# Kernel tuning notes

Hardware: AMD Instinct MI355X
Metric: run time of the kernel (lower is better)

## Reference

```python
import jax, jax.numpy as jnp
import numpy as np

H = 5  # hidden size of both LSTMs

def _lstm_layer(x, Wih, Whh, bih, bhh):
    """x: [B,T,I] -> hs: [B,T,H]. PyTorch gate order i,f,g,o; zero init state."""
    B, T, _ = x.shape
    # precompute input contribution for all timesteps: [T,B,4H]
    xg = (jnp.einsum('bti,gi->btg', x, Wih) + bih + bhh).transpose(1, 0, 2)
    def step(carry, xg_t):
        h, c = carry
        g = xg_t + h @ Whh.T
        i, f, gg, o = jnp.split(g, 4, axis=-1)
        c = jax.nn.sigmoid(f) * c + jax.nn.sigmoid(i) * jnp.tanh(gg)
        h = jax.nn.sigmoid(o) * jnp.tanh(c)
        return (h, c), h
    h0 = jnp.zeros((B, H), x.dtype)
    (_, _), hs = jax.lax.scan(step, (h0, h0), xg)
    return hs.transpose(1, 0, 2)  # [B,T,H]

def setup_inputs() -> dict:
    key = jax.random.key(0)
    ks = jax.random.split(key, 32)
    B, T = 16384, 128
    def u(k, shape, fan):
        s = 1.0 / np.sqrt(fan)
        return jax.random.uniform(k, shape, jnp.float32, -s, s)
    inp = {
        'x1': jax.random.normal(ks[0], (B, T, 5), jnp.float32),
        'x2': jax.random.normal(ks[1], (B, T, 5), jnp.float32),
        # lstm1 (1 layer)
        'Wih1': u(ks[2], (4*H, 5), H), 'Whh1': u(ks[3], (4*H, H), H),
        'bih1': u(ks[4], (4*H,), H), 'bhh1': u(ks[5], (4*H,), H),
        # lstm2 layer 0
        'Wih2a': u(ks[6], (4*H, 5), H), 'Whh2a': u(ks[7], (4*H, H), H),
        'bih2a': u(ks[8], (4*H,), H), 'bhh2a': u(ks[9], (4*H,), H),
        # lstm2 layer 1
        'Wih2b': u(ks[10], (4*H, H), H), 'Whh2b': u(ks[11], (4*H, H), H),
        'bih2b': u(ks[12], (4*H,), H), 'bhh2b': u(ks[13], (4*H,), H),
        # FC stack 20->32->32->16->16->5
        'W1': u(ks[14], (32, 20), 20), 'b1': u(ks[15], (32,), 20),
        'W2': u(ks[16], (32, 32), 32), 'b2': u(ks[17], (32,), 32),
        'W3': u(ks[18], (16, 32), 32), 'b3': u(ks[19], (16,), 32),
        'W4': u(ks[20], (16, 16), 16), 'b4': u(ks[21], (16,), 16),
        'W5': u(ks[22], (5, 16), 16), 'b5': u(ks[23], (5,), 16),
    }
    return inp

def reference(x1, x2, Wih1, Whh1, bih1, bhh1, Wih2a, Whh2a, bih2a, bhh2a,
              Wih2b, Whh2b, bih2b, bhh2b, W1, b1, W2, b2, W3, b3, W4, b4, W5, b5):
    out1 = _lstm_layer(x1, Wih1, Whh1, bih1, bhh1)[:, -1, :]            # [B,5]
    h2 = _lstm_layer(x2, Wih2a, Whh2a, bih2a, bhh2a)                    # [B,T,5]
    out2 = _lstm_layer(h2, Wih2b, Whh2b, bih2b, bhh2b)[:, -1, :]        # [B,5]
    out = jnp.concatenate([x1[:, -1, :], x2[:, -1, :], out1, out2], axis=1)  # [B,20]
    out = jax.nn.relu(out @ W1.T + b1)
    out = jax.nn.relu(out @ W2.T + b2)
    out = jax.nn.relu(out @ W3.T + b3)
    out = jax.nn.relu(out @ W4.T + b4)
    return out @ W5.T + b5  # [B,5]
```

## Files before the change

kernel.cpp:

```cpp
#include <hip/hip_runtime.h>

#define DEV __device__ __forceinline__
#define KSIG (-1.442695041f)
#define KTANH (-2.885390082f)

DEV float fexp2(float x) { return __builtin_amdgcn_exp2f(x); }
DEV float frcp(float x) { return __builtin_amdgcn_rcpf(x); }
DEV float bperm(int a, float x) {
  return __int_as_float(__builtin_amdgcn_ds_bpermute(a, __float_as_int(x)));
}

struct CellB {
  float w[4][10];
  float b[4];
};

DEV void load_cellB(CellB& W, int u, const float* __restrict__ Wih,
                    const float* __restrict__ Whh,
                    const float* __restrict__ bih,
                    const float* __restrict__ bhh) {
#pragma unroll
  for (int rt = 0; rt < 4; ++rt) {
    int row = 5 * rt + u;
    float kx = (rt == 2) ? KTANH : KSIG;
#pragma unroll
    for (int k = 0; k < 5; ++k) {
      W.w[rt][k] = kx * Wih[row * 5 + k];
      W.w[rt][5 + k] = kx * Whh[row * 5 + k];
    }
    W.b[rt] = kx * (bih[row] + bhh[row]);
  }
}

DEV void cellB_step(const CellB& W, const float xin[5], float hAll[5],
                    float& c, const int bp[5]) {
  float acc[4];
#pragma unroll
  for (int rt = 0; rt < 4; ++rt) {
    float a = W.b[rt];
#pragma unroll
    for (int k = 0; k < 5; ++k) a = fmaf(W.w[rt][k], xin[k], a);
#pragma unroll
    for (int k = 0; k < 5; ++k) a = fmaf(W.w[rt][5 + k], hAll[k], a);
    acc[rt] = a;
  }
  float gi = frcp(1.f + fexp2(acc[0]));
  float gf = frcp(1.f + fexp2(acc[1]));
  float gg = fmaf(2.f, frcp(1.f + fexp2(acc[2])), -1.f);
  float go = frcp(1.f + fexp2(acc[3]));
  c = fmaf(gf, c, gi * gg);
  float th = fmaf(2.f, frcp(1.f + fexp2(KTANH * c)), -1.f);
  float h = go * th;
#pragma unroll
  for (int u2 = 0; u2 < 5; ++u2) hAll[u2] = bperm(bp[u2], h);
}

__global__ __launch_bounds__(64, 2) void rnn5_kernel(
    const float* __restrict__ x1, const float* __restrict__ x2,
    const float* __restrict__ Wih1, const float* __restrict__ Whh1,
    const float* __restrict__ bih1, const float* __restrict__ bhh1,
    const float* __restrict__ Wih2a, const float* __restrict__ Whh2a,
    const float* __restrict__ bih2a, const float* __restrict__ bhh2a,
    const float* __restrict__ Wih2b, const float* __restrict__ Whh2b,
    const float* __restrict__ bih2b, const float* __restrict__ bhh2b,
    const float* __restrict__ W1, const float* __restrict__ b1,
    const float* __restrict__ W2, const float* __restrict__ b2,
    const float* __restrict__ W3, const float* __restrict__ b3,
    const float* __restrict__ W4, const float* __restrict__ b4,
    const float* __restrict__ W5, const float* __restrict__ b5,
    float* __restrict__ out, int B) {
  __shared__ float sIn[12][20];
  __shared__ float sA[12][32];
  __shared__ float sB[12][32];

  const int l = threadIdx.x;
  const int g = l / 5;
  const int u = l - 5 * g;
  const bool act = (g < 12);
  const int el = act ? g : 11;
  const int eg = blockIdx.x * 12 + el;
  const int egc = (eg < B) ? eg : (B - 1);

  CellB Wc0, Wc1, Wc2;
  load_cellB(Wc0, u, Wih1, Whh1, bih1, bhh1);
  load_cellB(Wc1, u, Wih2a, Whh2a, bih2a, bhh2a);
  load_cellB(Wc2, u, Wih2b, Whh2b, bih2b, bhh2b);

  int bp[5];
#pragma unroll
  for (int u2 = 0; u2 < 5; ++u2) bp[u2] = (5 * g + u2) * 4;

  const float* px1 = x1 + (size_t)egc * 640;
  const float* px2 = x2 + (size_t)egc * 640;

  float h1[5], h2a[5], h2b[5];
  float c1 = 0.f, c2 = 0.f, c3 = 0.f;
  float xa[5], xb[5];
#pragma unroll
  for (int k = 0; k < 5; ++k) {
    h1[k] = h2a[k] = h2b[k] = 0.f;
    xa[k] = px1[k];
    xb[k] = px2[k];
  }

  for (int t = 0; t < 128; ++t) {
    const int tn = (t < 127) ? t + 1 : 127;
    float na[5], nb[5];
#pragma unroll
    for (int k = 0; k < 5; ++k) {
      na[k] = px1[tn * 5 + k];
      nb[k] = px2[tn * 5 + k];
    }
    cellB_step(Wc0, xa, h1, c1, bp);
    cellB_step(Wc1, xb, h2a, c2, bp);
    cellB_step(Wc2, h2a, h2b, c3, bp);
#pragma unroll
    for (int k = 0; k < 5; ++k) {
      xa[k] = na[k];
      xb[k] = nb[k];
    }
  }

  if (act) {
    sIn[el][u] = xa[u];
    sIn[el][5 + u] = xb[u];
    sIn[el][10 + u] = h1[u];
    sIn[el][15 + u] = h2b[u];
  }
  __syncthreads();

  for (int task = l; task < 12 * 32; task += 64) {
    int e = task >> 5, n = task & 31;
    float acc = b1[n];
#pragma unroll
    for (int k = 0; k < 20; ++k) acc = fmaf(W1[n * 20 + k], sIn[e][k], acc);
    sA[e][n] = fmaxf(acc, 0.f);
  }
  __syncthreads();
  for (int task = l; task < 12 * 32; task += 64) {
    int e = task >> 5, n = task & 31;
    float acc = b2[n];
#pragma unroll
    for (int k = 0; k < 32; ++k) acc = fmaf(W2[n * 32 + k], sA[e][k], acc);
    sB[e][n] = fmaxf(acc, 0.f);
  }
  __syncthreads();
  for (int task = l; task < 12 * 16; task += 64) {
    int e = task >> 4, n = task & 15;
    float acc = b3[n];
#pragma unroll
    for (int k = 0; k < 32; ++k) acc = fmaf(W3[n * 32 + k], sB[e][k], acc);
    sA[e][n] = fmaxf(acc, 0.f);
  }
  __syncthreads();
  for (int task = l; task < 12 * 16; task += 64) {
    int e = task >> 4, n = task & 15;
    float acc = b4[n];
#pragma unroll
    for (int k = 0; k < 16; ++k) acc = fmaf(W4[n * 16 + k], sA[e][k], acc);
    sB[e][n] = fmaxf(acc, 0.f);
  }
  __syncthreads();
  if (l < 60) {
    int e = l / 5, n = l - 5 * (l / 5);
    float acc = b5[n];
#pragma unroll
    for (int k = 0; k < 16; ++k) acc = fmaf(W5[n * 16 + k], sB[e][k], acc);
    int ego = blockIdx.x * 12 + e;
    if (ego < B) out[(size_t)ego * 5 + n] = acc;
  }
}

extern "C" void kernel_launch(void* const* d_in, const int* in_sizes, int n_in,
                              void* d_out, int out_size, void* d_ws,
                              size_t ws_size, hipStream_t stream) {
  const float* x1 = (const float*)d_in[0];
  const float* x2 = (const float*)d_in[1];
  const float* Wih1 = (const float*)d_in[2];
  const float* Whh1 = (const float*)d_in[3];
  const float* bih1 = (const float*)d_in[4];
  const float* bhh1 = (const float*)d_in[5];
  const float* Wih2a = (const float*)d_in[6];
  const float* Whh2a = (const float*)d_in[7];
  const float* bih2a = (const float*)d_in[8];
  const float* bhh2a = (const float*)d_in[9];
  const float* Wih2b = (const float*)d_in[10];
  const float* Whh2b = (const float*)d_in[11];
  const float* bih2b = (const float*)d_in[12];
  const float* bhh2b = (const float*)d_in[13];
  const float* W1 = (const float*)d_in[14];
  const float* b1 = (const float*)d_in[15];
  const float* W2 = (const float*)d_in[16];
  const float* b2 = (const float*)d_in[17];
  const float* W3 = (const float*)d_in[18];
  const float* b3 = (const float*)d_in[19];
  const float* W4 = (const float*)d_in[20];
  const float* b4 = (const float*)d_in[21];
  const float* W5 = (const float*)d_in[22];
  const float* b5 = (const float*)d_in[23];

  int B = in_sizes[0] / 640;
  int blocks = (B + 11) / 12;

  rnn5_kernel<<<blocks, 64, 0, stream>>>(
      x1, x2, Wih1, Whh1, bih1, bhh1, Wih2a, Whh2a, bih2a, bhh2a, Wih2b, Whh2b,
      bih2b, bhh2b, W1, b1, W2, b2, W3, b3, W4, b4, W5, b5, (float*)d_out, B);
}
```

Measured before the change: 241.9 us.

## Split LSTM branches into separate blocks, use packed FMA, move FC to separate kernel

The fused recurrent kernel is split so one set of blocks runs the single-layer LSTM on x1 and another set runs the two-layer stack on x2. This doubles the block count and shortens the serial per-block chain to at most two cells per step. The gate dot products now use packed two-wide FMAs. The FC stack moves to a second kernel with one element per thread, passing hidden states through the output buffer and workspace. The cost is imbalance between the two block roles, an extra launch, and a global round trip for the hidden states. fc_kernel reads wsh1 from d_out while writing out, but each thread reads its own row before writing it.

```diff
diff --git a/kernel.cpp b/kernel.cpp
--- a/kernel.cpp
+++ b/kernel.cpp
@@ -3,19 +3,24 @@
 #define DEV __device__ __forceinline__
 #define KSIG (-1.442695041f)
 #define KTANH (-2.885390082f)
+
+typedef float f2 __attribute__((ext_vector_type(2)));
 
 DEV float fexp2(float x) { return __builtin_amdgcn_exp2f(x); }
 DEV float frcp(float x) { return __builtin_amdgcn_rcpf(x); }
 DEV float bperm(int a, float x) {
   return __int_as_float(__builtin_amdgcn_ds_bpermute(a, __float_as_int(x)));
 }
-
-struct CellB {
-  float w[4][10];
-  float b[4];
+DEV f2 pkfma(f2 a, f2 b, f2 c) { return __builtin_elementwise_fma(a, b, c); }
+
+struct CellP {
+  f2 wx[4][2];
+  f2 wh[4][2];
+  float wx4[4], wh4[4];
+  f2 b2[4];
 };
 
-DEV void load_cellB(CellB& W, int u, const float* __restrict__ Wih,
+DEV void load_cellP(CellP& W, int u, const float* __restrict__ Wih,
                     const float* __restrict__ Whh,
                     const float* __restrict__ bih,
                     const float* __restrict__ bhh) {
@@ -23,26 +28,30 @@
   for (int rt = 0; rt < 4; ++rt) {
     int row = 5 * rt + u;
     float kx = (rt == 2) ? KTANH : KSIG;
-#pragma unroll
-    for (int k = 0; k < 5; ++k) {
-      W.w[rt][k] = kx * Wih[row * 5 + k];
-      W.w[rt][5 + k] = kx * Whh[row * 5 + k];
-    }
-    W.b[rt] = kx * (bih[row] + bhh[row]);
-  }
-}
-
-DEV void cellB_step(const CellB& W, const float xin[5], float hAll[5],
-                    float& c, const int bp[5]) {
+    W.wx[rt][0] = (f2){kx * Wih[row * 5 + 0], kx * Wih[row * 5 + 1]};
+    W.wx[rt][1] = (f2){kx * Wih[row * 5 + 2], kx * Wih[row * 5 + 3]};
+    W.wx4[rt] = kx * Wih[row * 5 + 4];
+    W.wh[rt][0] = (f2){kx * Whh[row * 5 + 0], kx * Whh[row * 5 + 1]};
+    W.wh[rt][1] = (f2){kx * Whh[row * 5 + 2], kx * Whh[row * 5 + 3]};
+    W.wh4[rt] = kx * Whh[row * 5 + 4];
+    W.b2[rt] = (f2){kx * (bih[row] + bhh[row]), 0.f};
+  }
+}
+
+DEV void stepP(const CellP& W, const f2 xp[2], float x4, float hAll[5],
+               float& c, const int bp[5]) {
+  f2 hp0 = (f2){hAll[0], hAll[1]};
+  f2 hp1 = (f2){hAll[2], hAll[3]};
   float acc[4];
 #pragma unroll
   for (int rt = 0; rt < 4; ++rt) {
-    float a = W.b[rt];
-#pragma unroll
-    for (int k = 0; k < 5; ++k) a = fmaf(W.w[rt][k], xin[k], a);
-#pragma unroll
-    for (int k = 0; k < 5; ++k) a = fmaf(W.w[rt][5 + k], hAll[k], a);
-    acc[rt] = a;
+    f2 a2 = pkfma(W.wx[rt][0], xp[0], W.b2[rt]);
+    a2 = pkfma(W.wx[rt][1], xp[1], a2);
+    a2 = pkfma(W.wh[rt][0], hp0, a2);
+    a2 = pkfma(W.wh[rt][1], hp1, a2);
+    float a = a2.x + a2.y;
+    a = fmaf(W.wx4[rt], x4, a);
+    acc[rt] = fmaf(W.wh4[rt], hAll[4], a);
   }
   float gi = frcp(1.f + fexp2(acc[0]));
   float gf = frcp(1.f + fexp2(acc[1]));
@@ -55,7 +64,7 @@
   for (int u2 = 0; u2 < 5; ++u2) hAll[u2] = bperm(bp[u2], h);
 }
 
-__global__ __launch_bounds__(64, 2) void rnn5_kernel(
+__global__ __launch_bounds__(64, 2) void rnn_split_kernel(
     const float* __restrict__ x1, const float* __restrict__ x2,
     const float* __restrict__ Wih1, const float* __restrict__ Whh1,
     const float* __restrict__ bih1, const float* __restrict__ bhh1,
@@ -63,111 +72,130 @@
     const float* __restrict__ bih2a, const float* __restrict__ bhh2a,
     const float* __restrict__ Wih2b, const float* __restrict__ Whh2b,
     const float* __restrict__ bih2b, const float* __restrict__ bhh2b,
-    const float* __restrict__ W1, const float* __restrict__ b1,
-    const float* __restrict__ W2, const float* __restrict__ b2,
-    const float* __restrict__ W3, const float* __restrict__ b3,
-    const float* __restrict__ W4, const float* __restrict__ b4,
-    const float* __restrict__ W5, const float* __restrict__ b5,
-    float* __restrict__ out, int B) {
-  __shared__ float sIn[12][20];
-  __shared__ float sA[12][32];
-  __shared__ float sB[12][32];
-
+    float* __restrict__ h1out, float* __restrict__ h2out, int B, int nB) {
   const int l = threadIdx.x;
   const int g = l / 5;
   const int u = l - 5 * g;
   const bool act = (g < 12);
   const int el = act ? g : 11;
-  const int eg = blockIdx.x * 12 + el;
+  const bool roleB = (blockIdx.x < (unsigned)nB);
+  const int blk = roleB ? blockIdx.x : blockIdx.x - nB;
+  const int eg = blk * 12 + el;
   const int egc = (eg < B) ? eg : (B - 1);
 
-  CellB Wc0, Wc1, Wc2;
-  load_cellB(Wc0, u, Wih1, Whh1, bih1, bhh1);
-  load_cellB(Wc1, u, Wih2a, Whh2a, bih2a, bhh2a);
-  load_cellB(Wc2, u, Wih2b, Whh2b, bih2b, bhh2b);
-
   int bp[5];
 #pragma unroll
   for (int u2 = 0; u2 < 5; ++u2) bp[u2] = (5 * g + u2) * 4;
 
-  const float* px1 = x1 + (size_t)egc * 640;
-  const float* px2 = x2 + (size_t)egc * 640;
-
-  float h1[5], h2a[5], h2b[5];
-  float c1 = 0.f, c2 = 0.f, c3 = 0.f;
-  float xa[5], xb[5];
+  if (roleB) {
+    CellP Wa, Wb;
+    load_cellP(Wa, u, Wih2a, Whh2a, bih2a, bhh2a);
+    load_cellP(Wb, u, Wih2b, Whh2b, bih2b, bhh2b);
+    const float* px = x2 + (size_t)egc * 640;
+
+    float h2a[5], h2b[5];
+    float c2 = 0.f, c3 = 0.f;
+#pragma unroll
+    for (int k = 0; k < 5; ++k) h2a[k] = h2b[k] = 0.f;
+    f2 xp[2] = {(f2){px[0], px[1]}, (f2){px[2], px[3]}};
+    float x4 = px[4];
+
+    for (int t = 0; t < 128; ++t) {
+      const int tn = (t < 127) ? t + 1 : 127;
+      f2 n0 = (f2){px[tn * 5 + 0], px[tn * 5 + 1]};
+      f2 n1 = (f2){px[tn * 5 + 2], px[tn * 5 + 3]};
+      float n4 = px[tn * 5 + 4];
+      stepP(Wa, xp, x4, h2a, c2, bp);
+      f2 hp[2] = {(f2){h2a[0], h2a[1]}, (f2){h2a[2], h2a[3]}};
+      stepP(Wb, hp, h2a[4], h2b, c3, bp);
+      xp[0] = n0;
+      xp[1] = n1;
+      x4 = n4;
+    }
+    if (act && eg < B) h2out[(size_t)eg * 5 + u] = h2b[u];
+  } else {
+    CellP W0;
+    load_cellP(W0, u, Wih1, Whh1, bih1, bhh1);
+    const float* px = x1 + (size_t)egc * 640;
+
+    float h1[5];
+    float c1 = 0.f;
+#pragma unroll
+    for (int k = 0; k < 5; ++k) h1[k] = 0.f;
+    f2 xp[2] = {(f2){px[0], px[1]}, (f2){px[2], px[3]}};
+    float x4 = px[4];
+
+    for (int t = 0; t < 128; ++t) {
+      const int tn = (t < 127) ? t + 1 : 127;
+      f2 n0 = (f2){px[tn * 5 + 0], px[tn * 5 + 1]};
+      f2 n1 = (f2){px[tn * 5 + 2], px[tn * 5 + 3]};
+      float n4 = px[tn * 5 + 4];
+      stepP(W0, xp, x4, h1, c1, bp);
+      xp[0] = n0;
+      xp[1] = n1;
+      x4 = n4;
+    }
+    if (act && eg < B) h1out[(size_t)eg * 5 + u] = h1[u];
+  }
+}
+
+__global__ __launch_bounds__(64) void fc_kernel(
+    const float* __restrict__ x1, const float* __restrict__ x2,
+    const float* wsh1, const float* __restrict__ wsh2,
+    const float* __restrict__ W1, const float* __restrict__ b1,
+    const float* __restrict__ W2, const float* __restrict__ b2,
+    const float* __restrict__ W3, const float* __restrict__ b3,
+    const float* __restrict__ W4, const float* __restrict__ b4,
+    const float* __restrict__ W5, const float* __restrict__ b5, float* out,
+    int B) {
+  int e = blockIdx.x * 64 + threadIdx.x;
+  if (e >= B) return;
+  float in0[20];
 #pragma unroll
   for (int k = 0; k < 5; ++k) {
-    h1[k] = h2a[k] = h2b[k] = 0.f;
-    xa[k] = px1[k];
-    xb[k] = px2[k];
-  }
-
-  for (int t = 0; t < 128; ++t) {
-    const int tn = (t < 127) ? t + 1 : 127;
-    float na[5], nb[5];
-#pragma unroll
-    for (int k = 0; k < 5; ++k) {
-      na[k] = px1[tn * 5 + k];
-      nb[k] = px2[tn * 5 + k];
-    }
-    cellB_step(Wc0, xa, h1, c1, bp);
-    cellB_step(Wc1, xb, h2a, c2, bp);
-    cellB_step(Wc2, h2a, h2b, c3, bp);
-#pragma unroll
-    for (int k = 0; k < 5; ++k) {
-      xa[k] = na[k];
-      xb[k] = nb[k];
-    }
-  }
-
-  if (act) {
-    sIn[el][u] = xa[u];
-    sIn[el][5 + u] = xb[u];
-    sIn[el][10 + u] = h1[u];
-    sIn[el][15 + u] = h2b[u];
-  }
-  __syncthreads();
-
-  for (int task = l; task < 12 * 32; task += 64) {
-    int e = task >> 5, n = task & 31;
+    in0[k] = x1[(size_t)e * 640 + 635 + k];
+    in0[5 + k] = x2[(size_t)e * 640 + 635 + k];
+    in0[10 + k] = wsh1[(size_t)e * 5 + k];
+    in0[15 + k] = wsh2[(size_t)e * 5 + k];
+  }
+  float v1[32];
+#pragma unroll
+  for (int n = 0; n < 32; ++n) {
     float acc = b1[n];
 #pragma unroll
-    for (int k = 0; k < 20; ++k) acc = fmaf(W1[n * 20 + k], sIn[e][k], acc);
-    sA[e][n] = fmaxf(acc, 0.f);
-  }
-  __syncthreads();
-  for (int task = l; task < 12 * 32; task += 64) {
-    int e = task >> 5, n = task & 31;
+    for (int k = 0; k < 20; ++k) acc = fmaf(W1[n * 20 + k], in0[k], acc);
+    v1[n] = fmaxf(acc, 0.f);
+  }
+  float v2[32];
+#pragma unroll
+  for (int n = 0; n < 32; ++n) {
     float acc = b2[n];
 #pragma unroll
-    for (int k = 0; k < 32; ++k) acc = fmaf(W2[n * 32 + k], sA[e][k], acc);
-    sB[e][n] = fmaxf(acc, 0.f);
-  }
-  __syncthreads();
-  for (int task = l; task < 12 * 16; task += 64) {
-    int e = task >> 4, n = task & 15;
+    for (int k = 0; k < 32; ++k) acc = fmaf(W2[n * 32 + k], v1[k], acc);
+    v2[n] = fmaxf(acc, 0.f);
+  }
+  float v3[16];
+#pragma unroll
+  for (int n = 0; n < 16; ++n) {
     float acc = b3[n];
 #pragma unroll
-    for (int k = 0; k < 32; ++k) acc = fmaf(W3[n * 32 + k], sB[e][k], acc);
-    sA[e][n] = fmaxf(acc, 0.f);
-  }
-  __syncthreads();
-  for (int task = l; task < 12 * 16; task += 64) {
-    int e = task >> 4, n = task & 15;
+    for (int k = 0; k < 32; ++k) acc = fmaf(W3[n * 32 + k], v2[k], acc);
+    v3[n] = fmaxf(acc, 0.f);
+  }
+  float v4[16];
+#pragma unroll
+  for (int n = 0; n < 16; ++n) {
     float acc = b4[n];
 #pragma unroll
-    for (int k = 0; k < 16; ++k) acc = fmaf(W4[n * 16 + k], sA[e][k], acc);
-    sB[e][n] = fmaxf(acc, 0.f);
-  }
-  __syncthreads();
-  if (l < 60) {
-    int e = l / 5, n = l - 5 * (l / 5);
+    for (int k = 0; k < 16; ++k) acc = fmaf(W4[n * 16 + k], v3[k], acc);
+    v4[n] = fmaxf(acc, 0.f);
+  }
+#pragma unroll
+  for (int n = 0; n < 5; ++n) {
     float acc = b5[n];
 #pragma unroll
-    for (int k = 0; k < 16; ++k) acc = fmaf(W5[n * 16 + k], sB[e][k], acc);
-    int ego = blockIdx.x * 12 + e;
-    if (ego < B) out[(size_t)ego * 5 + n] = acc;
+    for (int k = 0; k < 16; ++k) acc = fmaf(W5[n * 16 + k], v4[k], acc);
+    out[(size_t)e * 5 + n] = acc;
   }
 }
 
@@ -200,9 +228,14 @@
   const float* b5 = (const float*)d_in[23];
 
   int B = in_sizes[0] / 640;
-  int blocks = (B + 11) / 12;
-
-  rnn5_kernel<<<blocks, 64, 0, stream>>>(
+  int nB = (B + 11) / 12;
+  float* wsh1 = (float*)d_out;
+  float* wsh2 = (float*)d_ws;
+
+  rnn_split_kernel<<<2 * nB, 64, 0, stream>>>(
       x1, x2, Wih1, Whh1, bih1, bhh1, Wih2a, Whh2a, bih2a, bhh2a, Wih2b, Whh2b,
-      bih2b, bhh2b, W1, b1, W2, b2, W3, b3, W4, b4, W5, b5, (float*)d_out, B);
-}
+      bih2b, bhh2b, wsh1, wsh2, B, nB);
+  fc_kernel<<<(B + 63) / 64, 64, 0, stream>>>(x1, x2, wsh1, wsh2, W1, b1, W2,
+                                              b2, W3, b3, W4, b4, W5, b5,
+                                              (float*)d_out, B);
+}
```

Measured after the change: 257.5 us. 1.06x slower.

## Split the three LSTM cells across three wavefronts and use packed FMA

Applied to the files above, without the earlier changes.

Each of the three LSTM cells now runs on its own wavefront inside a 192-thread block instead of one wave running all three in sequence. The second layer of lstm2 runs one step behind, reading h2a from a double-buffered shared array, with a __syncthreads after every timestep. The gate dot products now use packed 2-wide float FMAs. The aim is to shorten each wave's serial dependency chain and raise occupancy, at the cost of 128 block barriers and lockstep coupling between the waves.

```diff
diff --git a/kernel.cpp b/kernel.cpp
--- a/kernel.cpp
+++ b/kernel.cpp
@@ -3,19 +3,24 @@
 #define DEV __device__ __forceinline__
 #define KSIG (-1.442695041f)
 #define KTANH (-2.885390082f)
+
+typedef float f2 __attribute__((ext_vector_type(2)));
 
 DEV float fexp2(float x) { return __builtin_amdgcn_exp2f(x); }
 DEV float frcp(float x) { return __builtin_amdgcn_rcpf(x); }
 DEV float bperm(int a, float x) {
   return __int_as_float(__builtin_amdgcn_ds_bpermute(a, __float_as_int(x)));
 }
-
-struct CellB {
-  float w[4][10];
-  float b[4];
+DEV f2 pkfma(f2 a, f2 b, f2 c) { return __builtin_elementwise_fma(a, b, c); }
+
+struct CellP {
+  f2 wx[4][2];
+  f2 wh[4][2];
+  float wx4[4], wh4[4];
+  f2 b2[4];
 };
 
-DEV void load_cellB(CellB& W, int u, const float* __restrict__ Wih,
+DEV void load_cellP(CellP& W, int u, const float* __restrict__ Wih,
                     const float* __restrict__ Whh,
                     const float* __restrict__ bih,
                     const float* __restrict__ bhh) {
@@ -23,26 +28,30 @@
   for (int rt = 0; rt < 4; ++rt) {
     int row = 5 * rt + u;
     float kx = (rt == 2) ? KTANH : KSIG;
-#pragma unroll
-    for (int k = 0; k < 5; ++k) {
-      W.w[rt][k] = kx * Wih[row * 5 + k];
-      W.w[rt][5 + k] = kx * Whh[row * 5 + k];
-    }
-    W.b[rt] = kx * (bih[row] + bhh[row]);
-  }
-}
-
-DEV void cellB_step(const CellB& W, const float xin[5], float hAll[5],
-                    float& c, const int bp[5]) {
+    W.wx[rt][0] = (f2){kx * Wih[row * 5 + 0], kx * Wih[row * 5 + 1]};
+    W.wx[rt][1] = (f2){kx * Wih[row * 5 + 2], kx * Wih[row * 5 + 3]};
+    W.wx4[rt] = kx * Wih[row * 5 + 4];
+    W.wh[rt][0] = (f2){kx * Whh[row * 5 + 0], kx * Whh[row * 5 + 1]};
+    W.wh[rt][1] = (f2){kx * Whh[row * 5 + 2], kx * Whh[row * 5 + 3]};
+    W.wh4[rt] = kx * Whh[row * 5 + 4];
+    W.b2[rt] = (f2){kx * (bih[row] + bhh[row]), 0.f};
+  }
+}
+
+DEV float stepP(const CellP& W, const f2 xp[2], float x4, float hAll[5],
+                float& c, const int bp[5]) {
+  f2 hp0 = (f2){hAll[0], hAll[1]};
+  f2 hp1 = (f2){hAll[2], hAll[3]};
   float acc[4];
 #pragma unroll
   for (int rt = 0; rt < 4; ++rt) {
-    float a = W.b[rt];
-#pragma unroll
-    for (int k = 0; k < 5; ++k) a = fmaf(W.w[rt][k], xin[k], a);
-#pragma unroll
-    for (int k = 0; k < 5; ++k) a = fmaf(W.w[rt][5 + k], hAll[k], a);
-    acc[rt] = a;
+    f2 a2 = pkfma(W.wx[rt][0], xp[0], W.b2[rt]);
+    a2 = pkfma(W.wx[rt][1], xp[1], a2);
+    a2 = pkfma(W.wh[rt][0], hp0, a2);
+    a2 = pkfma(W.wh[rt][1], hp1, a2);
+    float a = a2.x + a2.y;
+    a = fmaf(W.wx4[rt], x4, a);
+    acc[rt] = fmaf(W.wh4[rt], hAll[4], a);
   }
   float gi = frcp(1.f + fexp2(acc[0]));
   float gf = frcp(1.f + fexp2(acc[1]));
@@ -53,9 +62,10 @@
   float h = go * th;
 #pragma unroll
   for (int u2 = 0; u2 < 5; ++u2) hAll[u2] = bperm(bp[u2], h);
-}
-
-__global__ __launch_bounds__(64, 2) void rnn5_kernel(
+  return h;
+}
+
+__global__ __launch_bounds__(192, 4) void rnn3w_kernel(
     const float* __restrict__ x1, const float* __restrict__ x2,
     const float* __restrict__ Wih1, const float* __restrict__ Whh1,
     const float* __restrict__ bih1, const float* __restrict__ bhh1,
@@ -69,11 +79,14 @@
     const float* __restrict__ W4, const float* __restrict__ b4,
     const float* __restrict__ W5, const float* __restrict__ b5,
     float* __restrict__ out, int B) {
+  __shared__ float sH[2][64];
   __shared__ float sIn[12][20];
   __shared__ float sA[12][32];
   __shared__ float sB[12][32];
 
-  const int l = threadIdx.x;
+  const int tid = threadIdx.x;
+  const int w = tid >> 6;
+  const int l = tid & 63;
   const int g = l / 5;
   const int u = l - 5 * g;
   const bool act = (g < 12);
@@ -81,55 +94,85 @@
   const int eg = blockIdx.x * 12 + el;
   const int egc = (eg < B) ? eg : (B - 1);
 
-  CellB Wc0, Wc1, Wc2;
-  load_cellB(Wc0, u, Wih1, Whh1, bih1, bhh1);
-  load_cellB(Wc1, u, Wih2a, Whh2a, bih2a, bhh2a);
-  load_cellB(Wc2, u, Wih2b, Whh2b, bih2b, bhh2b);
+  CellP W;
+  if (w == 0)
+    load_cellP(W, u, Wih1, Whh1, bih1, bhh1);
+  else if (w == 1)
+    load_cellP(W, u, Wih2a, Whh2a, bih2a, bhh2a);
+  else
+    load_cellP(W, u, Wih2b, Whh2b, bih2b, bhh2b);
 
   int bp[5];
 #pragma unroll
   for (int u2 = 0; u2 < 5; ++u2) bp[u2] = (5 * g + u2) * 4;
 
-  const float* px1 = x1 + (size_t)egc * 640;
-  const float* px2 = x2 + (size_t)egc * 640;
-
-  float h1[5], h2a[5], h2b[5];
-  float c1 = 0.f, c2 = 0.f, c3 = 0.f;
-  float xa[5], xb[5];
-#pragma unroll
-  for (int k = 0; k < 5; ++k) {
-    h1[k] = h2a[k] = h2b[k] = 0.f;
-    xa[k] = px1[k];
-    xb[k] = px2[k];
-  }
+  const float* px = ((w == 0) ? x1 : x2) + (size_t)egc * 640;
+
+  if (tid < 128) sH[tid >> 6][tid & 63] = 0.f;
+
+  float hAll[5];
+  float c = 0.f, hOwn = 0.f;
+#pragma unroll
+  for (int k = 0; k < 5; ++k) hAll[k] = 0.f;
+
+  f2 xp[2];
+  float x4 = 0.f;
+  if (w < 2) {
+    xp[0] = (f2){px[0], px[1]};
+    xp[1] = (f2){px[2], px[3]};
+    x4 = px[4];
+  }
+  __syncthreads();
 
   for (int t = 0; t < 128; ++t) {
-    const int tn = (t < 127) ? t + 1 : 127;
-    float na[5], nb[5];
-#pragma unroll
-    for (int k = 0; k < 5; ++k) {
-      na[k] = px1[tn * 5 + k];
-      nb[k] = px2[tn * 5 + k];
-    }
-    cellB_step(Wc0, xa, h1, c1, bp);
-    cellB_step(Wc1, xb, h2a, c2, bp);
-    cellB_step(Wc2, h2a, h2b, c3, bp);
-#pragma unroll
-    for (int k = 0; k < 5; ++k) {
-      xa[k] = na[k];
-      xb[k] = nb[k];
-    }
+    f2 xin[2];
+    float xin4;
+    if (w == 2) {
+      const float* s = &sH[(t + 1) & 1][g * 5];
+      xin[0] = (f2){s[0], s[1]};
+      xin[1] = (f2){s[2], s[3]};
+      xin4 = s[4];
+    } else {
+      xin[0] = xp[0];
+      xin[1] = xp[1];
+      xin4 = x4;
+    }
+    if (w < 2) {
+      const int tn = (t < 127) ? t + 1 : 127;
+      xp[0] = (f2){px[tn * 5 + 0], px[tn * 5 + 1]};
+      xp[1] = (f2){px[tn * 5 + 2], px[tn * 5 + 3]};
+      x4 = px[tn * 5 + 4];
+    }
+    hOwn = stepP(W, xin, xin4, hAll, c, bp);
+    if (w == 2 && t == 0) {
+#pragma unroll
+      for (int k = 0; k < 5; ++k) hAll[k] = 0.f;
+      c = 0.f;
+      hOwn = 0.f;
+    }
+    if (w == 1 && act) sH[t & 1][g * 5 + u] = hOwn;
+    __syncthreads();
+  }
+
+  if (w == 2) {
+    const float* s = &sH[1][g * 5];
+    f2 xin[2] = {(f2){s[0], s[1]}, (f2){s[2], s[3]}};
+    hOwn = stepP(W, xin, s[4], hAll, c, bp);
   }
 
   if (act) {
-    sIn[el][u] = xa[u];
-    sIn[el][5 + u] = xb[u];
-    sIn[el][10 + u] = h1[u];
-    sIn[el][15 + u] = h2b[u];
-  }
-  __syncthreads();
-
-  for (int task = l; task < 12 * 32; task += 64) {
+    if (w == 0) {
+      sIn[el][u] = x1[(size_t)egc * 640 + 635 + u];
+      sIn[el][10 + u] = hOwn;
+    } else if (w == 1) {
+      sIn[el][5 + u] = x2[(size_t)egc * 640 + 635 + u];
+    } else {
+      sIn[el][15 + u] = hOwn;
+    }
+  }
+  __syncthreads();
+
+  for (int task = tid; task < 12 * 32; task += 192) {
     int e = task >> 5, n = task & 31;
     float acc = b1[n];
 #pragma unroll
@@ -137,7 +180,7 @@
     sA[e][n] = fmaxf(acc, 0.f);
   }
   __syncthreads();
-  for (int task = l; task < 12 * 32; task += 64) {
+  for (int task = tid; task < 12 * 32; task += 192) {
     int e = task >> 5, n = task & 31;
     float acc = b2[n];
 #pragma unroll
@@ -145,24 +188,24 @@
     sB[e][n] = fmaxf(acc, 0.f);
   }
   __syncthreads();
-  for (int task = l; task < 12 * 16; task += 64) {
-    int e = task >> 4, n = task & 15;
+  {
+    int e = tid >> 4, n = tid & 15;
     float acc = b3[n];
 #pragma unroll
     for (int k = 0; k < 32; ++k) acc = fmaf(W3[n * 32 + k], sB[e][k], acc);
     sA[e][n] = fmaxf(acc, 0.f);
   }
   __syncthreads();
-  for (int task = l; task < 12 * 16; task += 64) {
-    int e = task >> 4, n = task & 15;
+  {
+    int e = tid >> 4, n = tid & 15;
     float acc = b4[n];
 #pragma unroll
     for (int k = 0; k < 16; ++k) acc = fmaf(W4[n * 16 + k], sA[e][k], acc);
     sB[e][n] = fmaxf(acc, 0.f);
   }
   __syncthreads();
-  if (l < 60) {
-    int e = l / 5, n = l - 5 * (l / 5);
+  if (tid < 60) {
+    int e = tid / 5, n = tid - 5 * (tid / 5);
     float acc = b5[n];
 #pragma unroll
     for (int k = 0; k < 16; ++k) acc = fmaf(W5[n * 16 + k], sB[e][k], acc);
@@ -200,9 +243,9 @@
   const float* b5 = (const float*)d_in[23];
 
   int B = in_sizes[0] / 640;
-  int blocks = (B + 11) / 12;
-
-  rnn5_kernel<<<blocks, 64, 0, stream>>>(
+  int nB = (B + 11) / 12;
+
+  rnn3w_kernel<<<nB, 192, 0, stream>>>(
       x1, x2, Wih1, Whh1, bih1, bhh1, Wih2a, Whh2a, bih2a, bhh2a, Wih2b, Whh2b,
       bih2b, bhh2b, W1, b1, W2, b2, W3, b3, W4, b4, W5, b5, (float*)d_out, B);
 }
```

Result: faster. 224.3 us (-7.3%).

## Remap LSTM work to 4 lanes per sequence, one gate type per lane

Applied to the files above, without the earlier changes.

Each wavefront now handles 16 sequences with 4 lanes per sequence; each lane computes one gate type for all 5 hidden units. Gates are exchanged across the 4-lane quad with DPP broadcasts instead of ds_bpermute, so every lane holds the full hidden state without LDS round trips. Dot products use packed 2-wide FMAs, and 16 lanes now fill the wave instead of 60 of 64. The trade-off is redundant cell/tanh computation across the 4 lanes and higher register pressure, with launch bounds lowered to 1 block per CU hint.

```diff
diff --git a/kernel.cpp b/kernel.cpp
--- a/kernel.cpp
+++ b/kernel.cpp
@@ -4,58 +4,94 @@
 #define KSIG (-1.442695041f)
 #define KTANH (-2.885390082f)
 
+typedef float f2 __attribute__((ext_vector_type(2)));
+
 DEV float fexp2(float x) { return __builtin_amdgcn_exp2f(x); }
 DEV float frcp(float x) { return __builtin_amdgcn_rcpf(x); }
-DEV float bperm(int a, float x) {
-  return __int_as_float(__builtin_amdgcn_ds_bpermute(a, __float_as_int(x)));
-}
-
-struct CellB {
-  float w[4][10];
-  float b[4];
+DEV f2 pkfma(f2 a, f2 b, f2 c) { return __builtin_elementwise_fma(a, b, c); }
+
+template <int S>
+DEV float qb(float x) {
+  int i = __builtin_amdgcn_update_dpp(0, __float_as_int(x), S * 0x55, 0xF, 0xF,
+                                      true);
+  return __int_as_float(i);
+}
+
+struct CellQ {
+  f2 wx01[5], wx23[5], wh01[5], wh23[5];
+  float wx4[5], wh4[5], b[5];
 };
 
-DEV void load_cellB(CellB& W, int u, const float* __restrict__ Wih,
+DEV void load_cellQ(CellQ& W, int s, const float* __restrict__ Wih,
                     const float* __restrict__ Whh,
                     const float* __restrict__ bih,
                     const float* __restrict__ bhh) {
-#pragma unroll
-  for (int rt = 0; rt < 4; ++rt) {
-    int row = 5 * rt + u;
-    float kx = (rt == 2) ? KTANH : KSIG;
-#pragma unroll
-    for (int k = 0; k < 5; ++k) {
-      W.w[rt][k] = kx * Wih[row * 5 + k];
-      W.w[rt][5 + k] = kx * Whh[row * 5 + k];
-    }
-    W.b[rt] = kx * (bih[row] + bhh[row]);
-  }
-}
-
-DEV void cellB_step(const CellB& W, const float xin[5], float hAll[5],
-                    float& c, const int bp[5]) {
-  float acc[4];
-#pragma unroll
-  for (int rt = 0; rt < 4; ++rt) {
-    float a = W.b[rt];
-#pragma unroll
-    for (int k = 0; k < 5; ++k) a = fmaf(W.w[rt][k], xin[k], a);
-#pragma unroll
-    for (int k = 0; k < 5; ++k) a = fmaf(W.w[rt][5 + k], hAll[k], a);
-    acc[rt] = a;
-  }
-  float gi = frcp(1.f + fexp2(acc[0]));
-  float gf = frcp(1.f + fexp2(acc[1]));
-  float gg = fmaf(2.f, frcp(1.f + fexp2(acc[2])), -1.f);
-  float go = frcp(1.f + fexp2(acc[3]));
-  c = fmaf(gf, c, gi * gg);
-  float th = fmaf(2.f, frcp(1.f + fexp2(KTANH * c)), -1.f);
-  float h = go * th;
-#pragma unroll
-  for (int u2 = 0; u2 < 5; ++u2) hAll[u2] = bperm(bp[u2], h);
-}
-
-__global__ __launch_bounds__(64, 2) void rnn5_kernel(
+  const float kx = (s == 2) ? KTANH : KSIG;
+#pragma unroll
+  for (int j = 0; j < 5; ++j) {
+    const int row = 5 * s + j;
+    W.wx01[j] = (f2){kx * Wih[row * 5 + 0], kx * Wih[row * 5 + 1]};
+    W.wx23[j] = (f2){kx * Wih[row * 5 + 2], kx * Wih[row * 5 + 3]};
+    W.wx4[j] = kx * Wih[row * 5 + 4];
+    W.wh01[j] = (f2){kx * Whh[row * 5 + 0], kx * Whh[row * 5 + 1]};
+    W.wh23[j] = (f2){kx * Whh[row * 5 + 2], kx * Whh[row * 5 + 3]};
+    W.wh4[j] = kx * Whh[row * 5 + 4];
+    W.b[j] = kx * (bih[row] + bhh[row]);
+  }
+}
+
+struct StateQ {
+  f2 hp01, hp23;
+  float h4;
+  float c[5];
+};
+
+DEV void zeroQ(StateQ& st) {
+  st.hp01 = (f2){0.f, 0.f};
+  st.hp23 = (f2){0.f, 0.f};
+  st.h4 = 0.f;
+#pragma unroll
+  for (int j = 0; j < 5; ++j) st.c[j] = 0.f;
+}
+
+DEV void stepQ(const CellQ& W, f2 x01, f2 x23, float x4, StateQ& st, float m2,
+               float a2) {
+  float a[5];
+#pragma unroll
+  for (int j = 0; j < 5; ++j) {
+    f2 acc2 = pkfma(W.wx01[j], x01, (f2){W.b[j], 0.f});
+    acc2 = pkfma(W.wx23[j], x23, acc2);
+    acc2 = pkfma(W.wh01[j], st.hp01, acc2);
+    acc2 = pkfma(W.wh23[j], st.hp23, acc2);
+    float acc = acc2.x + acc2.y;
+    acc = fmaf(W.wx4[j], x4, acc);
+    acc = fmaf(W.wh4[j], st.h4, acc);
+    a[j] = fmaf(m2, frcp(1.f + fexp2(acc)), a2);
+  }
+#pragma unroll
+  for (int j = 0; j < 5; ++j) {
+    float I = qb<0>(a[j]);
+    float F = qb<1>(a[j]);
+    float G = qb<2>(a[j]);
+    float O = qb<3>(a[j]);
+    float cj = fmaf(F, st.c[j], I * G);
+    st.c[j] = cj;
+    float th = fmaf(2.f, frcp(1.f + fexp2(KTANH * cj)), -1.f);
+    float h = O * th;
+    if (j == 0)
+      st.hp01.x = h;
+    else if (j == 1)
+      st.hp01.y = h;
+    else if (j == 2)
+      st.hp23.x = h;
+    else if (j == 3)
+      st.hp23.y = h;
+    else
+      st.h4 = h;
+  }
+}
+
+__global__ __launch_bounds__(64, 1) void rnnq_kernel(
     const float* __restrict__ x1, const float* __restrict__ x2,
     const float* __restrict__ Wih1, const float* __restrict__ Whh1,
     const float* __restrict__ bih1, const float* __restrict__ bhh1,
@@ -69,105 +105,141 @@
     const float* __restrict__ W4, const float* __restrict__ b4,
     const float* __restrict__ W5, const float* __restrict__ b5,
     float* __restrict__ out, int B) {
-  __shared__ float sIn[12][20];
-  __shared__ float sA[12][32];
-  __shared__ float sB[12][32];
+  __shared__ float sIn[16][20];
+  __shared__ float sA[16][32];
+  __shared__ float sBf[16][32];
 
   const int l = threadIdx.x;
-  const int g = l / 5;
-  const int u = l - 5 * g;
-  const bool act = (g < 12);
-  const int el = act ? g : 11;
-  const int eg = blockIdx.x * 12 + el;
+  const int e = l >> 2;
+  const int s = l & 3;
+  const int eg = blockIdx.x * 16 + e;
   const int egc = (eg < B) ? eg : (B - 1);
 
-  CellB Wc0, Wc1, Wc2;
-  load_cellB(Wc0, u, Wih1, Whh1, bih1, bhh1);
-  load_cellB(Wc1, u, Wih2a, Whh2a, bih2a, bhh2a);
-  load_cellB(Wc2, u, Wih2b, Whh2b, bih2b, bhh2b);
-
-  int bp[5];
-#pragma unroll
-  for (int u2 = 0; u2 < 5; ++u2) bp[u2] = (5 * g + u2) * 4;
+  CellQ Wc1, Wc2a, Wc2b;
+  load_cellQ(Wc1, s, Wih1, Whh1, bih1, bhh1);
+  load_cellQ(Wc2a, s, Wih2a, Whh2a, bih2a, bhh2a);
+  load_cellQ(Wc2b, s, Wih2b, Whh2b, bih2b, bhh2b);
+
+  const float m2 = (s == 2) ? 2.f : 1.f;
+  const float a2 = (s == 2) ? -1.f : 0.f;
 
   const float* px1 = x1 + (size_t)egc * 640;
   const float* px2 = x2 + (size_t)egc * 640;
 
-  float h1[5], h2a[5], h2b[5];
-  float c1 = 0.f, c2 = 0.f, c3 = 0.f;
-  float xa[5], xb[5];
-#pragma unroll
-  for (int k = 0; k < 5; ++k) {
-    h1[k] = h2a[k] = h2b[k] = 0.f;
-    xa[k] = px1[k];
-    xb[k] = px2[k];
-  }
+  StateQ s1, s2a, s2b;
+  zeroQ(s1);
+  zeroQ(s2a);
+  zeroQ(s2b);
+
+  f2 xa01 = (f2){px1[0], px1[1]}, xa23 = (f2){px1[2], px1[3]};
+  float xa4 = px1[4];
+  f2 xb01 = (f2){px2[0], px2[1]}, xb23 = (f2){px2[2], px2[3]};
+  float xb4 = px2[4];
 
   for (int t = 0; t < 128; ++t) {
     const int tn = (t < 127) ? t + 1 : 127;
-    float na[5], nb[5];
-#pragma unroll
-    for (int k = 0; k < 5; ++k) {
-      na[k] = px1[tn * 5 + k];
-      nb[k] = px2[tn * 5 + k];
-    }
-    cellB_step(Wc0, xa, h1, c1, bp);
-    cellB_step(Wc1, xb, h2a, c2, bp);
-    cellB_step(Wc2, h2a, h2b, c3, bp);
-#pragma unroll
-    for (int k = 0; k < 5; ++k) {
-      xa[k] = na[k];
-      xb[k] = nb[k];
-    }
-  }
-
-  if (act) {
-    sIn[el][u] = xa[u];
-    sIn[el][5 + u] = xb[u];
-    sIn[el][10 + u] = h1[u];
-    sIn[el][15 + u] = h2b[u];
-  }
-  __syncthreads();
-
-  for (int task = l; task < 12 * 32; task += 64) {
-    int e = task >> 5, n = task & 31;
-    float acc = b1[n];
-#pragma unroll
-    for (int k = 0; k < 20; ++k) acc = fmaf(W1[n * 20 + k], sIn[e][k], acc);
-    sA[e][n] = fmaxf(acc, 0.f);
-  }
-  __syncthreads();
-  for (int task = l; task < 12 * 32; task += 64) {
-    int e = task >> 5, n = task & 31;
-    float acc = b2[n];
-#pragma unroll
-    for (int k = 0; k < 32; ++k) acc = fmaf(W2[n * 32 + k], sA[e][k], acc);
-    sB[e][n] = fmaxf(acc, 0.f);
-  }
-  __syncthreads();
-  for (int task = l; task < 12 * 16; task += 64) {
-    int e = task >> 4, n = task & 15;
-    float acc = b3[n];
-#pragma unroll
-    for (int k = 0; k < 32; ++k) acc = fmaf(W3[n * 32 + k], sB[e][k], acc);
-    sA[e][n] = fmaxf(acc, 0.f);
-  }
-  __syncthreads();
-  for (int task = l; task < 12 * 16; task += 64) {
-    int e = task >> 4, n = task & 15;
-    float acc = b4[n];
-#pragma unroll
-    for (int k = 0; k < 16; ++k) acc = fmaf(W4[n * 16 + k], sA[e][k], acc);
-    sB[e][n] = fmaxf(acc, 0.f);
-  }
-  __syncthreads();
-  if (l < 60) {
-    int e = l / 5, n = l - 5 * (l / 5);
-    float acc = b5[n];
-#pragma unroll
-    for (int k = 0; k < 16; ++k) acc = fmaf(W5[n * 16 + k], sB[e][k], acc);
-    int ego = blockIdx.x * 12 + e;
-    if (ego < B) out[(size_t)ego * 5 + n] = acc;
+    f2 na01 = (f2){px1[tn * 5 + 0], px1[tn * 5 + 1]};
+    f2 na23 = (f2){px1[tn * 5 + 2], px1[tn * 5 + 3]};
+    float na4 = px1[tn * 5 + 4];
+    f2 nb01 = (f2){px2[tn * 5 + 0], px2[tn * 5 + 1]};
+    f2 nb23 = (f2){px2[tn * 5 + 2], px2[tn * 5 + 3]};
+    float nb4 = px2[tn * 5 + 4];
+
+    stepQ(Wc2a, xb01, xb23, xb4, s2a, m2, a2);
+    stepQ(Wc1, xa01, xa23, xa4, s1, m2, a2);
+    stepQ(Wc2b, s2a.hp01, s2a.hp23, s2a.h4, s2b, m2, a2);
+
+    xa01 = na01;
+    xa23 = na23;
+    xa4 = na4;
+    xb01 = nb01;
+    xb23 = nb23;
+    xb4 = nb4;
+  }
+
+  if (s == 0) {
+    sIn[e][0] = xa01.x;
+    sIn[e][1] = xa01.y;
+    sIn[e][2] = xa23.x;
+    sIn[e][3] = xa23.y;
+    sIn[e][4] = xa4;
+    sIn[e][5] = xb01.x;
+    sIn[e][6] = xb01.y;
+    sIn[e][7] = xb23.x;
+    sIn[e][8] = xb23.y;
+    sIn[e][9] = xb4;
+    sIn[e][10] = s1.hp01.x;
+    sIn[e][11] = s1.hp01.y;
+    sIn[e][12] = s1.hp23.x;
+    sIn[e][13] = s1.hp23.y;
+    sIn[e][14] = s1.h4;
+    sIn[e][15] = s2b.hp01.x;
+    sIn[e][16] = s2b.hp01.y;
+    sIn[e][17] = s2b.hp23.x;
+    sIn[e][18] = s2b.hp23.y;
+    sIn[e][19] = s2b.h4;
+  }
+  __syncthreads();
+
+  {
+    const int n = l & 31;
+#pragma unroll
+    for (int r = 0; r < 8; ++r) {
+      int ei = (l >> 5) + 2 * r;
+      float acc = b1[n];
+#pragma unroll
+      for (int k = 0; k < 20; ++k) acc = fmaf(W1[n * 20 + k], sIn[ei][k], acc);
+      sA[ei][n] = fmaxf(acc, 0.f);
+    }
+  }
+  __syncthreads();
+  {
+    const int n = l & 31;
+#pragma unroll
+    for (int r = 0; r < 8; ++r) {
+      int ei = (l >> 5) + 2 * r;
+      float acc = b2[n];
+#pragma unroll
+      for (int k = 0; k < 32; ++k) acc = fmaf(W2[n * 32 + k], sA[ei][k], acc);
+      sBf[ei][n] = fmaxf(acc, 0.f);
+    }
+  }
+  __syncthreads();
+  {
+    const int n = l & 15;
+#pragma unroll
+    for (int r = 0; r < 4; ++r) {
+      int ei = (l >> 4) + 4 * r;
+      float acc = b3[n];
+#pragma unroll
+      for (int k = 0; k < 32; ++k) acc = fmaf(W3[n * 32 + k], sBf[ei][k], acc);
+      sA[ei][n] = fmaxf(acc, 0.f);
+    }
+  }
+  __syncthreads();
+  {
+    const int n = l & 15;
+#pragma unroll
+    for (int r = 0; r < 4; ++r) {
+      int ei = (l >> 4) + 4 * r;
+      float acc = b4[n];
+#pragma unroll
+      for (int k = 0; k < 16; ++k) acc = fmaf(W4[n * 16 + k], sA[ei][k], acc);
+      sBf[ei][n] = fmaxf(acc, 0.f);
+    }
+  }
+  __syncthreads();
+#pragma unroll
+  for (int r = 0; r < 2; ++r) {
+    int task = l + 64 * r;
+    if (task < 80) {
+      int ei = task / 5, n = task - 5 * (task / 5);
+      float acc = b5[n];
+#pragma unroll
+      for (int k = 0; k < 16; ++k) acc = fmaf(W5[n * 16 + k], sBf[ei][k], acc);
+      int ego = blockIdx.x * 16 + ei;
+      if (ego < B) out[(size_t)ego * 5 + n] = acc;
+    }
   }
 }
 
@@ -200,9 +272,9 @@
   const float* b5 = (const float*)d_in[23];
 
   int B = in_sizes[0] / 640;
-  int blocks = (B + 11) / 12;
-
-  rnn5_kernel<<<blocks, 64, 0, stream>>>(
+  int nB = (B + 15) / 16;
+
+  rnnq_kernel<<<nB, 64, 0, stream>>>(
       x1, x2, Wih1, Whh1, bih1, bhh1, Wih2a, Whh2a, bih2a, bhh2a, Wih2b, Whh2b,
       bih2b, bhh2b, W1, b1, W2, b2, W3, b3, W4, b4, W5, b5, (float*)d_out, B);
 }
```

New measurement: 260.3 us. 1.08x slower.
